# Optimization experiments

Measured on AMD Instinct MI355X. Metric: run time of the kernel, lower is better.

The kernel has to match this reference:

```python
import jax, jax.numpy as jnp
import numpy as np

N_NODES = 100000
N_EDGES = 1600000
HIDDEN = 128
N_LAYERS = 3
N_GRAPHS = 100
EPS = 1e-5


def setup_inputs() -> dict:
    key = jax.random.key(0)
    ks = jax.random.split(key, 9)
    node = jax.random.normal(ks[0], (N_NODES, HIDDEN), dtype=jnp.float32)
    edge_index = jax.random.randint(ks[1], (2, N_EDGES), 0, N_NODES, dtype=jnp.int32)
    edge_attr = jax.random.uniform(ks[2], (N_EDGES,), dtype=jnp.float32)
    batch_ptr = jnp.sort(jax.random.randint(ks[3], (N_NODES,), 0, N_GRAPHS, dtype=jnp.int32))
    W = jax.random.normal(ks[4], (N_LAYERS, HIDDEN, HIDDEN), dtype=jnp.float32) * (1.0 / np.sqrt(HIDDEN))
    b = jax.random.normal(ks[5], (N_LAYERS, HIDDEN), dtype=jnp.float32) * 0.02
    gn_weight = jnp.ones((N_LAYERS, HIDDEN), dtype=jnp.float32)
    gn_bias = jnp.zeros((N_LAYERS, HIDDEN), dtype=jnp.float32)
    gn_alpha = jnp.ones((N_LAYERS, HIDDEN), dtype=jnp.float32)
    return {"node": node, "edge_index": edge_index, "edge_attr": edge_attr,
            "batch_ptr": batch_ptr, "W": W, "b": b, "gn_weight": gn_weight,
            "gn_bias": gn_bias, "gn_alpha": gn_alpha}


def reference(node, edge_index, edge_attr, batch_ptr, W, b, gn_weight, gn_bias, gn_alpha):
    N, d = node.shape
    src, dst = edge_index[0], edge_index[1]
    # GCN normalization with self-loops (weight 1), as in PyG gcn_norm
    loop = jnp.arange(N, dtype=src.dtype)
    src_a = jnp.concatenate([src, loop])
    dst_a = jnp.concatenate([dst, loop])
    w_a = jnp.concatenate([edge_attr, jnp.ones((N,), dtype=edge_attr.dtype)])
    deg = jax.ops.segment_sum(w_a, dst_a, num_segments=N)
    dis = jnp.where(deg > 0, deg ** -0.5, 0.0)
    norm = dis[src_a] * w_a * dis[dst_a]  # [E+N]

    counts = jax.ops.segment_sum(jnp.ones((N,), node.dtype), batch_ptr,
                                 num_segments=N_GRAPHS)[:, None]  # [G,1]

    for l in range(W.shape[0]):
        # GCNConv: linear transform, then gather-normalize-scatter over edges
        h = node @ W[l]  # [N,d]
        agg = jax.ops.segment_sum(norm[:, None] * h[src_a], dst_a, num_segments=N) + b[l]
        # GraphNorm: per-graph mean shift (scaled by alpha) and variance norm
        mean = jax.ops.segment_sum(agg, batch_ptr, num_segments=N_GRAPHS) / counts  # [G,d]
        sub = agg - gn_alpha[l] * mean[batch_ptr]
        var = jax.ops.segment_sum(sub * sub, batch_ptr, num_segments=N_GRAPHS) / counts
        node = jax.nn.relu(gn_weight[l] * sub * jax.lax.rsqrt(var[batch_ptr] + EPS) + gn_bias[l])
    return node
```

## Files before the change

### kernel.cpp

```cpp
#include <hip/hip_runtime.h>
#include <cstdint>

#define N_N 100000
#define N_E 1600000
#define HID 128
#define N_G 100
#define EPSF 1e-5f

#define NB   256
#define EPB  ((N_E + NB - 1) / NB)
#define NBKT ((N_N + 255) >> 8)

static inline int ceil_div(int a, int b){ return (a + b - 1) / b; }

typedef __attribute__((ext_vector_type(8))) short bf16x8;
typedef __attribute__((ext_vector_type(4))) float f32x4;

__device__ inline float bf2f(unsigned short u){
  return __uint_as_float(((unsigned int)u) << 16);
}
__device__ inline unsigned short f2bf(float f){
  unsigned int u = __float_as_uint(f);
  unsigned int r = u + 0x7fffu + ((u >> 16) & 1u);
  return (unsigned short)(r >> 16);
}
__device__ inline void fma8(float* acc, float nv, uint4 u){
  acc[0] += nv * __uint_as_float(u.x << 16);
  acc[1] += nv * __uint_as_float(u.x & 0xffff0000u);
  acc[2] += nv * __uint_as_float(u.y << 16);
  acc[3] += nv * __uint_as_float(u.y & 0xffff0000u);
  acc[4] += nv * __uint_as_float(u.z << 16);
  acc[5] += nv * __uint_as_float(u.z & 0xffff0000u);
  acc[6] += nv * __uint_as_float(u.w << 16);
  acc[7] += nv * __uint_as_float(u.w & 0xffff0000u);
}

__global__ void k_wt3(const float* __restrict__ W, unsigned short* __restrict__ Wt,
                      float* __restrict__ counts, float* __restrict__ sum,
                      float* __restrict__ sumsq){
  int i = blockIdx.x * 256 + threadIdx.x;
  if (i < N_G) counts[i] = 0.0f;
  if (i < N_G * HID){ sum[i] = 0.f; sumsq[i] = 0.f; }
  if (i >= 3 * HID * HID) return;
  int l = i >> 14;
  int r = i & 16383;
  int n = r >> 7, k = r & 127;
  Wt[i] = f2bf(W[l * HID * HID + k * HID + n]);
}

__global__ void k_counts(const int* __restrict__ bp, float* __restrict__ counts){
  int t = blockIdx.x * 256 + threadIdx.x;
  int r0 = t * 32;
  if (r0 >= N_N) return;
  int r1 = min(r0 + 32, N_N);
  int curg = bp[r0];
  float acc = 0.f;
  for (int r = r0; r < r1; ++r){
    int g = bp[r];
    if (g != curg){ atomicAdd(&counts[curg], acc); acc = 0.f; curg = g; }
    acc += 1.0f;
  }
  atomicAdd(&counts[curg], acc);
}

__global__ __launch_bounds__(256) void k_hist(const int* __restrict__ dst,
                                              int* __restrict__ counts){
  __shared__ int h[NBKT];
  int t = threadIdx.x, blk = blockIdx.x;
  for (int i = t; i < NBKT; i += 256) h[i] = 0;
  __syncthreads();
  int e0 = blk * EPB, e1 = min(e0 + EPB, N_E);
  for (int e = e0 + t; e < e1; e += 256)
    atomicAdd(&h[dst[e] >> 8], 1);
  __syncthreads();
  for (int i = t; i < NBKT; i += 256) counts[i * NB + blk] = h[i];
}

__global__ __launch_bounds__(256) void k_scanA(int* __restrict__ data,
                                               int* __restrict__ bsum, int n){
  __shared__ int s[256];
  int t = threadIdx.x;
  int i = blockIdx.x * 256 + t;
  int v = (i < n) ? data[i] : 0;
  s[t] = v; __syncthreads();
  #pragma unroll
  for (int off = 1; off < 256; off <<= 1){
    int tmp = (t >= off) ? s[t - off] : 0;
    __syncthreads();
    s[t] += tmp;
    __syncthreads();
  }
  if (i < n) data[i] = s[t] - v;
  if (t == 255) bsum[blockIdx.x] = s[255];
}

__global__ __launch_bounds__(512) void k_scanB(int* __restrict__ bsum, int nblocks){
  __shared__ int s[512];
  int t = threadIdx.x;
  int v = (t < nblocks) ? bsum[t] : 0;
  s[t] = v; __syncthreads();
  #pragma unroll
  for (int off = 1; off < 512; off <<= 1){
    int tmp = (t >= off) ? s[t - off] : 0;
    __syncthreads();
    s[t] += tmp;
    __syncthreads();
  }
  if (t < nblocks) bsum[t] = s[t] - v;
}

__global__ void k_scanC(int* __restrict__ data, const int* __restrict__ bsum, int n){
  int i = blockIdx.x * 256 + threadIdx.x;
  if (i < n) data[i] += bsum[blockIdx.x];
}

__global__ __launch_bounds__(256) void k_part(const int* __restrict__ src,
                                              const int* __restrict__ dst,
                                              const float* __restrict__ w,
                                              const int* __restrict__ coff,
                                              int2* __restrict__ part){
  __shared__ int off[NBKT];
  int t = threadIdx.x, blk = blockIdx.x;
  for (int i = t; i < NBKT; i += 256) off[i] = coff[i * NB + blk];
  __syncthreads();
  int e0 = blk * EPB, e1 = min(e0 + EPB, N_E);
  for (int e = e0 + t; e < e1; e += 256){
    int d = dst[e];
    int pos = atomicAdd(&off[d >> 8], 1);
    part[pos] = make_int2(src[e] | ((d & 255) << 24), __float_as_int(w[e]));
  }
}

__global__ __launch_bounds__(256) void k_csr(const int* __restrict__ coff,
                                             const int2* __restrict__ part,
                                             int2* __restrict__ edge8,
                                             int* __restrict__ ptr,
                                             float* __restrict__ dis,
                                             float* __restrict__ nself){
  __shared__ int h[256];
  __shared__ int c[256];
  __shared__ float wsum[256];
  __shared__ int s[256];
  int t = threadIdx.x, b = blockIdx.x;
  int base  = coff[b * NB];
  int base2 = (b + 1 < NBKT) ? coff[(b + 1) * NB] : N_E;
  h[t] = 0; c[t] = 0; wsum[t] = 0.f;
  __syncthreads();
  for (int e = base + t; e < base2; e += 256){
    int2 v = part[e];
    int local = ((unsigned int)v.x) >> 24;
    atomicAdd(&h[local], 1);
    atomicAdd(&wsum[local], __int_as_float(v.y));
  }
  __syncthreads();
  int v0 = h[t];
  s[t] = v0; __syncthreads();
  #pragma unroll
  for (int off = 1; off < 256; off <<= 1){
    int tmp = (t >= off) ? s[t - off] : 0;
    __syncthreads();
    s[t] += tmp;
    __syncthreads();
  }
  int mybase = base + s[t] - v0;
  int node = (b << 8) + t;
  float dv = rsqrtf(1.0f + wsum[t]);
  if (node < N_N){
    ptr[node] = mybase;
    dis[node] = dv;
    nself[node] = dv * dv;
  }
  if (b == NBKT - 1 && t == 0) ptr[N_N] = N_E;
  h[t] = mybase;
  __syncthreads();
  wsum[t] = dv;
  __syncthreads();
  for (int e = base + t; e < base2; e += 256){
    int2 v = part[e];
    int local = ((unsigned int)v.x) >> 24;
    int pos = h[local] + atomicAdd(&c[local], 1);
    edge8[pos] = make_int2(v.x & 0x00ffffff,
                           __float_as_int(__int_as_float(v.y) * wsum[local]));
  }
}

__global__ void k_ne(const float* __restrict__ dis, int2* __restrict__ edge8){
  int e = blockIdx.x * 256 + threadIdx.x;
  if (e >= N_E) return;
  int2 v = edge8[e];
  v.y = __float_as_int(__int_as_float(v.y) * dis[v.x]);
  edge8[e] = v;
}

__global__ __launch_bounds__(256) void k_gemm(const float* __restrict__ X,
                                              const float* __restrict__ agg,
                                              int fused,
                                              const int* __restrict__ bp,
                                              const float* __restrict__ mean,
                                              const float* __restrict__ rstd,
                                              const float* __restrict__ alpha,
                                              const float* __restrict__ gwv,
                                              const float* __restrict__ gbv,
                                              const unsigned short* __restrict__ Wt,
                                              unsigned short* __restrict__ Hb, int nrows){
  __shared__ unsigned short lA[64 * 136];
  __shared__ unsigned short lB[128 * 136];
  int tid = threadIdx.x;
  int row0 = blockIdx.x * 64;

  #pragma unroll
  for (int i = 0; i < 8; ++i){
    int c = tid + i * 256;
    int r = c >> 4, cc = c & 15;
    *(uint4*)&lB[r * 136 + cc * 8] = ((const uint4*)Wt)[c];
  }
  #pragma unroll
  for (int i = 0; i < 8; ++i){
    int c = tid + i * 256;
    int r = c >> 5, cc = c & 31;
    int gr = row0 + r;
    float4 v = make_float4(0.f, 0.f, 0.f, 0.f);
    if (gr < nrows){
      if (!fused){
        v = *(const float4*)(X + (size_t)gr * HID + cc * 4);
      } else {
        int g = bp[gr];
        float4 a  = *(const float4*)(agg  + (size_t)gr * HID + cc * 4);
        float4 m  = *(const float4*)(mean + g * HID + cc * 4);
        float4 rs = *(const float4*)(rstd + g * HID + cc * 4);
        float4 al = *(const float4*)(alpha + cc * 4);
        float4 wv = *(const float4*)(gwv + cc * 4);
        float4 bv = *(const float4*)(gbv + cc * 4);
        v.x = fmaxf(wv.x * (a.x - al.x * m.x) * rs.x + bv.x, 0.f);
        v.y = fmaxf(wv.y * (a.y - al.y * m.y) * rs.y + bv.y, 0.f);
        v.z = fmaxf(wv.z * (a.z - al.z * m.z) * rs.z + bv.z, 0.f);
        v.w = fmaxf(wv.w * (a.w - al.w * m.w) * rs.w + bv.w, 0.f);
      }
    }
    unsigned short pk[4] = {f2bf(v.x), f2bf(v.y), f2bf(v.z), f2bf(v.w)};
    *(uint2*)&lA[r * 136 + cc * 4] = *(const uint2*)pk;
  }
  __syncthreads();

  int wave = tid >> 6;
  int lane = tid & 63;
  int l16 = lane & 15;
  int quad = lane >> 4;
  int am = wave * 16 + l16;

  bf16x8 afr[4];
  #pragma unroll
  for (int kc = 0; kc < 4; ++kc)
    afr[kc] = *(const bf16x8*)&lA[am * 136 + kc * 32 + quad * 8];

  #pragma unroll
  for (int nt = 0; nt < 8; ++nt){
    f32x4 acc = {0.f, 0.f, 0.f, 0.f};
    int bn = nt * 16 + l16;
    #pragma unroll
    for (int kc = 0; kc < 4; ++kc){
      bf16x8 bfr = *(const bf16x8*)&lB[bn * 136 + kc * 32 + quad * 8];
      acc = __builtin_amdgcn_mfma_f32_16x16x32_bf16(afr[kc], bfr, acc, 0, 0, 0);
    }
    int gr = row0 + wave * 16 + quad * 4;
    #pragma unroll
    for (int r = 0; r < 4; ++r){
      if (gr + r < nrows)
        Hb[(size_t)(gr + r) * HID + nt * 16 + l16] = f2bf(acc[r]);
    }
  }
}

__global__ __launch_bounds__(256) void k_gather(const int* __restrict__ ptr,
                                                const int2* __restrict__ edge8,
                                                const unsigned short* __restrict__ Hb,
                                                const float* __restrict__ nself,
                                                const float* __restrict__ bias,
                                                float* __restrict__ agg){
  int t = blockIdx.x * 256 + threadIdx.x;
  int node = t >> 4;
  if (node >= N_N) return;
  int lane = t & 15;
  const uint4* h16 = (const uint4*)Hb;
  float ns = nself[node];
  uint4 hu = h16[(size_t)node * 16 + lane];
  float4 b0 = ((const float4*)bias)[lane * 2];
  float4 b1 = ((const float4*)bias)[lane * 2 + 1];
  float acc[8] = {b0.x, b0.y, b0.z, b0.w, b1.x, b1.y, b1.z, b1.w};
  fma8(acc, ns, hu);

  int e0 = ptr[node], e1 = ptr[node + 1];
  int e = e0;
  for (; e + 4 <= e1; e += 4){
    int2 ev0 = edge8[e + 0];
    int2 ev1 = edge8[e + 1];
    int2 ev2 = edge8[e + 2];
    int2 ev3 = edge8[e + 3];
    uint4 r0 = h16[(size_t)ev0.x * 16 + lane];
    uint4 r1 = h16[(size_t)ev1.x * 16 + lane];
    uint4 r2 = h16[(size_t)ev2.x * 16 + lane];
    uint4 r3 = h16[(size_t)ev3.x * 16 + lane];
    fma8(acc, __int_as_float(ev0.y), r0);
    fma8(acc, __int_as_float(ev1.y), r1);
    fma8(acc, __int_as_float(ev2.y), r2);
    fma8(acc, __int_as_float(ev3.y), r3);
  }
  for (; e < e1; ++e){
    int2 ev = edge8[e];
    uint4 r0 = h16[(size_t)ev.x * 16 + lane];
    fma8(acc, __int_as_float(ev.y), r0);
  }
  float4* ap = (float4*)(agg + (size_t)node * HID + lane * 8);
  ap[0] = make_float4(acc[0], acc[1], acc[2], acc[3]);
  ap[1] = make_float4(acc[4], acc[5], acc[6], acc[7]);
}


__global__ __launch_bounds__(128) void k_gstat(const float* __restrict__ agg,
                                               const int* __restrict__ bp,
                                               float* __restrict__ sum,
                                               float* __restrict__ sumsq){
  int f = threadIdx.x;
  int r0 = blockIdx.x * 64;
  int r1 = min(r0 + 64, N_N);
  int curg = bp[r0];
  float s = 0.f, s2 = 0.f;
  for (int r = r0; r < r1; ++r){
    int g = bp[r];
    if (g != curg){
      atomicAdd(&sum[curg * HID + f], s);
      atomicAdd(&sumsq[curg * HID + f], s2);
      s = 0.f; s2 = 0.f; curg = g;
    }
    float v = agg[(size_t)r * HID + f];
    s += v; s2 += v * v;
  }
  atomicAdd(&sum[curg * HID + f], s);
  atomicAdd(&sumsq[curg * HID + f], s2);
}

__global__ void k_finstat(float* __restrict__ sum, float* __restrict__ sumsq,
                          const float* __restrict__ counts, const float* __restrict__ alpha,
                          float* __restrict__ mean, float* __restrict__ rstd){
  int i = blockIdx.x * 256 + threadIdx.x;
  if (i >= N_G * HID) return;
  int f = i & (HID - 1);
  float c = counts[i >> 7];
  float inv = c > 0.f ? 1.0f / c : 0.f;
  float m = sum[i] * inv;
  float ex2 = sumsq[i] * inv;
  float al = alpha[f];
  float var = ex2 - m * m * al * (2.0f - al);
  mean[i] = m;
  rstd[i] = rsqrtf(var + EPSF);
  sum[i] = 0.f;
  sumsq[i] = 0.f;
}

__global__ void k_out(const float* __restrict__ agg, const int* __restrict__ bp,
                      const float* __restrict__ mean, const float* __restrict__ rstd,
                      const float* __restrict__ alpha, const float* __restrict__ gw,
                      const float* __restrict__ gb, float* __restrict__ out){
  int idx = blockIdx.x * 256 + threadIdx.x;
  if (idx >= N_N * 32) return;
  int i = idx >> 5, q = idx & 31;
  int g = bp[i];
  float4 a  = ((const float4*)agg)[idx];
  float4 m  = ((const float4*)mean)[g * 32 + q];
  float4 r  = ((const float4*)rstd)[g * 32 + q];
  float4 al = ((const float4*)alpha)[q];
  float4 wv = ((const float4*)gw)[q];
  float4 bv = ((const float4*)gb)[q];
  float4 o;
  o.x = fmaxf(wv.x * (a.x - al.x * m.x) * r.x + bv.x, 0.f);
  o.y = fmaxf(wv.y * (a.y - al.y * m.y) * r.y + bv.y, 0.f);
  o.z = fmaxf(wv.z * (a.z - al.z * m.z) * r.z + bv.z, 0.f);
  o.w = fmaxf(wv.w * (a.w - al.w * m.w) * r.w + bv.w, 0.f);
  ((float4*)out)[idx] = o;
}


extern "C" void kernel_launch(void* const* d_in, const int* in_sizes, int n_in,
                              void* d_out, int out_size, void* d_ws, size_t ws_size,
                              hipStream_t stream){
  const float* node0 = (const float*)d_in[0];
  const int*   eidx  = (const int*)d_in[1];
  const float* eattr = (const float*)d_in[2];
  const int*   bp    = (const int*)d_in[3];
  const float* W     = (const float*)d_in[4];
  const float* bias  = (const float*)d_in[5];
  const float* gw    = (const float*)d_in[6];
  const float* gb    = (const float*)d_in[7];
  const float* ga    = (const float*)d_in[8];
  float* out = (float*)d_out;
  const int* src = eidx;
  const int* dst = eidx + N_E;

  char* p = (char*)d_ws;
  auto carve = [&](size_t nbytes) -> char* {
    char* q = p; p += (nbytes + 255) & ~(size_t)255; return q;
  };
  float* dis    = (float*)carve((size_t)N_N * 4);
  float* nself  = (float*)carve((size_t)N_N * 4);
  float* counts = (float*)carve((size_t)N_G * 4);
  int*   coff   = (int*)  carve((size_t)NBKT * NB * 4);
  int*   bsum   = (int*)  carve((size_t)512 * 4);
  int*   ptr    = (int*)  carve((size_t)(N_N + 1) * 4);
  int2*  edge8  = (int2*) carve((size_t)N_E * 8);
  unsigned short* hb = (unsigned short*)carve((size_t)N_N * HID * 2);
  unsigned short* wt = (unsigned short*)carve((size_t)3 * HID * HID * 2);
  float* agg    = (float*)carve((size_t)N_N * HID * 4);
  float* mean   = (float*)carve((size_t)N_G * HID * 4);
  float* rstd   = (float*)carve((size_t)N_G * HID * 4);
  float* sum    = (float*)carve((size_t)N_G * HID * 4);
  float* sumsq  = (float*)carve((size_t)N_G * HID * 4);
  int2*  part   = (int2*)agg;

  int nscan = NBKT * NB;
  int nscan_blocks = ceil_div(nscan, 256);

  k_wt3   <<<ceil_div(3 * HID * HID, 256), 256, 0, stream>>>(W, wt, counts, sum, sumsq);
  k_counts<<<ceil_div(N_N, 32 * 256), 256, 0, stream>>>(bp, counts);
  k_hist  <<<NB, 256, 0, stream>>>(dst, coff);
  k_scanA <<<nscan_blocks, 256, 0, stream>>>(coff, bsum, nscan);
  k_scanB <<<1, 512, 0, stream>>>(bsum, nscan_blocks);
  k_scanC <<<nscan_blocks, 256, 0, stream>>>(coff, bsum, nscan);
  k_part  <<<NB, 256, 0, stream>>>(src, dst, eattr, coff, part);
  k_csr   <<<NBKT, 256, 0, stream>>>(coff, part, edge8, ptr, dis, nself);
  k_ne    <<<ceil_div(N_E, 256), 256, 0, stream>>>(dis, edge8);

  for (int l = 0; l < 3; ++l){
    if (l == 0){
      k_gemm <<<ceil_div(N_N, 64), 256, 0, stream>>>(node0, nullptr, 0,
                 nullptr, nullptr, nullptr, nullptr, nullptr, nullptr,
                 wt, hb, N_N);
    } else {
      k_gemm <<<ceil_div(N_N, 64), 256, 0, stream>>>(nullptr, agg, 1,
                 bp, mean, rstd, ga + (l - 1) * HID, gw + (l - 1) * HID,
                 gb + (l - 1) * HID, wt + (size_t)l * HID * HID, hb, N_N);
    }
    k_gather <<<ceil_div(N_N * 16, 256), 256, 0, stream>>>(ptr, edge8, hb, nself,
                 bias + l * HID, agg);
    k_gstat  <<<ceil_div(N_N, 64), 128, 0, stream>>>(agg, bp, sum, sumsq);
    k_finstat<<<ceil_div(N_G * HID, 256), 256, 0, stream>>>(sum, sumsq, counts,
                 ga + l * HID, mean, rstd);
  }
  k_out <<<ceil_div(N_N * 32, 256), 256, 0, stream>>>(agg, bp, mean, rstd,
             ga + 2 * HID, gw + 2 * HID, gb + 2 * HID, out);
}
```

Baseline: 574.5 us.

## Slice H by feature columns per XCC and use persistent atomic-ticket gather

```diff
diff --git a/kernel.cpp b/kernel.cpp
--- a/kernel.cpp
+++ b/kernel.cpp
@@ -11,14 +11,15 @@
 #define EPB  ((N_E + NB - 1) / NB)
 #define NBKT ((N_N + 255) >> 8)
 
+#define NSL  8
+#define CHK  128
+#define NCH  ((N_N + CHK - 1) / CHK)
+
 static inline int ceil_div(int a, int b){ return (a + b - 1) / b; }
 
 typedef __attribute__((ext_vector_type(8))) short bf16x8;
 typedef __attribute__((ext_vector_type(4))) float f32x4;
 
-__device__ inline float bf2f(unsigned short u){
-  return __uint_as_float(((unsigned int)u) << 16);
-}
 __device__ inline unsigned short f2bf(float f){
   unsigned int u = __float_as_uint(f);
   unsigned int r = u + 0x7fffu + ((u >> 16) & 1u);
@@ -35,11 +36,18 @@
   acc[7] += nv * __uint_as_float(u.w & 0xffff0000u);
 }
 
+__device__ inline int get_xcc(){
+  unsigned x;
+  asm volatile("s_getreg_b32 %0, hwreg(HW_REG_XCC_ID)" : "=s"(x));
+  return (int)(x & (NSL - 1));
+}
+
 __global__ void k_wt3(const float* __restrict__ W, unsigned short* __restrict__ Wt,
                       float* __restrict__ counts, float* __restrict__ sum,
-                      float* __restrict__ sumsq){
+                      float* __restrict__ sumsq, int* __restrict__ tick){
   int i = blockIdx.x * 256 + threadIdx.x;
   if (i < N_G) counts[i] = 0.0f;
+  if (i < 3 * NSL) tick[i] = 0;
   if (i < N_G * HID){ sum[i] = 0.f; sumsq[i] = 0.f; }
   if (i >= 3 * HID * HID) return;
   int l = i >> 14;
@@ -263,56 +271,74 @@
       acc = __builtin_amdgcn_mfma_f32_16x16x32_bf16(afr[kc], bfr, acc, 0, 0, 0);
     }
     int gr = row0 + wave * 16 + quad * 4;
+    unsigned short* hbs = Hb + (size_t)nt * ((size_t)N_N * 16);
     #pragma unroll
     for (int r = 0; r < 4; ++r){
       if (gr + r < nrows)
-        Hb[(size_t)(gr + r) * HID + nt * 16 + l16] = f2bf(acc[r]);
-    }
-  }
-}
-
-__global__ __launch_bounds__(256) void k_gather(const int* __restrict__ ptr,
-                                                const int2* __restrict__ edge8,
-                                                const unsigned short* __restrict__ Hb,
-                                                const float* __restrict__ nself,
-                                                const float* __restrict__ bias,
-                                                float* __restrict__ agg){
-  int t = blockIdx.x * 256 + threadIdx.x;
-  int node = t >> 4;
-  if (node >= N_N) return;
-  int lane = t & 15;
-  const uint4* h16 = (const uint4*)Hb;
-  float ns = nself[node];
-  uint4 hu = h16[(size_t)node * 16 + lane];
-  float4 b0 = ((const float4*)bias)[lane * 2];
-  float4 b1 = ((const float4*)bias)[lane * 2 + 1];
-  float acc[8] = {b0.x, b0.y, b0.z, b0.w, b1.x, b1.y, b1.z, b1.w};
-  fma8(acc, ns, hu);
-
-  int e0 = ptr[node], e1 = ptr[node + 1];
-  int e = e0;
-  for (; e + 4 <= e1; e += 4){
-    int2 ev0 = edge8[e + 0];
-    int2 ev1 = edge8[e + 1];
-    int2 ev2 = edge8[e + 2];
-    int2 ev3 = edge8[e + 3];
-    uint4 r0 = h16[(size_t)ev0.x * 16 + lane];
-    uint4 r1 = h16[(size_t)ev1.x * 16 + lane];
-    uint4 r2 = h16[(size_t)ev2.x * 16 + lane];
-    uint4 r3 = h16[(size_t)ev3.x * 16 + lane];
-    fma8(acc, __int_as_float(ev0.y), r0);
-    fma8(acc, __int_as_float(ev1.y), r1);
-    fma8(acc, __int_as_float(ev2.y), r2);
-    fma8(acc, __int_as_float(ev3.y), r3);
-  }
-  for (; e < e1; ++e){
-    int2 ev = edge8[e];
-    uint4 r0 = h16[(size_t)ev.x * 16 + lane];
-    fma8(acc, __int_as_float(ev.y), r0);
-  }
-  float4* ap = (float4*)(agg + (size_t)node * HID + lane * 8);
-  ap[0] = make_float4(acc[0], acc[1], acc[2], acc[3]);
-  ap[1] = make_float4(acc[4], acc[5], acc[6], acc[7]);
+        hbs[(size_t)(gr + r) * 16 + l16] = f2bf(acc[r]);
+    }
+  }
+}
+
+__global__ __launch_bounds__(256, 8) void k_gather(const int* __restrict__ ptr,
+                                                   const int2* __restrict__ edge8,
+                                                   const unsigned short* __restrict__ Hb,
+                                                   const float* __restrict__ nself,
+                                                   const float* __restrict__ bias,
+                                                   float* __restrict__ agg,
+                                                   int* __restrict__ tick){
+  __shared__ int schunk;
+  int myx = get_xcc();
+  int half = threadIdx.x & 1;
+  int trow = threadIdx.x >> 1;
+  const long long* ep = (const long long*)edge8;
+  for (int ss = 0; ss < NSL; ++ss){
+    int s = (myx + ss) & (NSL - 1);
+    const uint4* hs = (const uint4*)(Hb + (size_t)s * ((size_t)N_N * 16));
+    float4 b0 = ((const float4*)bias)[s * 4 + half * 2];
+    float4 b1 = ((const float4*)bias)[s * 4 + half * 2 + 1];
+    for (;;){
+      if (threadIdx.x == 0) schunk = atomicAdd(&tick[s], 1);
+      __syncthreads();
+      int chunk = schunk;
+      __syncthreads();
+      if (chunk >= NCH) break;
+      int node = chunk * CHK + trow;
+      if (node < N_N){
+        float ns = __builtin_nontemporal_load(nself + node);
+        uint4 hu = hs[(size_t)node * 2 + half];
+        float acc[8] = {b0.x, b0.y, b0.z, b0.w, b1.x, b1.y, b1.z, b1.w};
+        fma8(acc, ns, hu);
+        int e0 = __builtin_nontemporal_load(ptr + node);
+        int e1 = __builtin_nontemporal_load(ptr + node + 1);
+        int e = e0;
+        for (; e + 4 <= e1; e += 4){
+          long long v0 = __builtin_nontemporal_load(ep + e + 0);
+          long long v1 = __builtin_nontemporal_load(ep + e + 1);
+          long long v2 = __builtin_nontemporal_load(ep + e + 2);
+          long long v3 = __builtin_nontemporal_load(ep + e + 3);
+          uint4 r0 = hs[(size_t)(unsigned int)v0 * 2 + half];
+          uint4 r1 = hs[(size_t)(unsigned int)v1 * 2 + half];
+          uint4 r2 = hs[(size_t)(unsigned int)v2 * 2 + half];
+          uint4 r3 = hs[(size_t)(unsigned int)v3 * 2 + half];
+          fma8(acc, __uint_as_float((unsigned int)(((unsigned long long)v0) >> 32)), r0);
+          fma8(acc, __uint_as_float((unsigned int)(((unsigned long long)v1) >> 32)), r1);
+          fma8(acc, __uint_as_float((unsigned int)(((unsigned long long)v2) >> 32)), r2);
+          fma8(acc, __uint_as_float((unsigned int)(((unsigned long long)v3) >> 32)), r3);
+        }
+        for (; e < e1; ++e){
+          long long v = __builtin_nontemporal_load(ep + e);
+          uint4 r0 = hs[(size_t)(unsigned int)v * 2 + half];
+          fma8(acc, __uint_as_float((unsigned int)(((unsigned long long)v) >> 32)), r0);
+        }
+        float* ap = agg + (size_t)node * HID + s * 16 + half * 8;
+        f32x4 w0 = {acc[0], acc[1], acc[2], acc[3]};
+        f32x4 w1 = {acc[4], acc[5], acc[6], acc[7]};
+        __builtin_nontemporal_store(w0, (f32x4*)ap);
+        __builtin_nontemporal_store(w1, (f32x4*)ap + 1);
+      }
+    }
+  }
 }
 
 
@@ -406,6 +432,7 @@
   int*   coff   = (int*)  carve((size_t)NBKT * NB * 4);
   int*   bsum   = (int*)  carve((size_t)512 * 4);
   int*   ptr    = (int*)  carve((size_t)(N_N + 1) * 4);
+  int*   tick   = (int*)  carve((size_t)3 * NSL * 4);
   int2*  edge8  = (int2*) carve((size_t)N_E * 8);
   unsigned short* hb = (unsigned short*)carve((size_t)N_N * HID * 2);
   unsigned short* wt = (unsigned short*)carve((size_t)3 * HID * HID * 2);
@@ -419,7 +446,7 @@
   int nscan = NBKT * NB;
   int nscan_blocks = ceil_div(nscan, 256);
 
-  k_wt3   <<<ceil_div(3 * HID * HID, 256), 256, 0, stream>>>(W, wt, counts, sum, sumsq);
+  k_wt3   <<<ceil_div(3 * HID * HID, 256), 256, 0, stream>>>(W, wt, counts, sum, sumsq, tick);
   k_counts<<<ceil_div(N_N, 32 * 256), 256, 0, stream>>>(bp, counts);
   k_hist  <<<NB, 256, 0, stream>>>(dst, coff);
   k_scanA <<<nscan_blocks, 256, 0, stream>>>(coff, bsum, nscan);
@@ -439,8 +466,8 @@
                  bp, mean, rstd, ga + (l - 1) * HID, gw + (l - 1) * HID,
                  gb + (l - 1) * HID, wt + (size_t)l * HID * HID, hb, N_N);
     }
-    k_gather <<<ceil_div(N_N * 16, 256), 256, 0, stream>>>(ptr, edge8, hb, nself,
-                 bias + l * HID, agg);
+    k_gather <<<2048, 256, 0, stream>>>(ptr, edge8, hb, nself,
+                 bias + l * HID, agg, tick + l * NSL);
     k_gstat  <<<ceil_div(N_N, 64), 128, 0, stream>>>(agg, bp, sum, sumsq);
     k_finstat<<<ceil_div(N_G * HID, 256), 256, 0, stream>>>(sum, sumsq, counts,
                  ga + l * HID, mean, rstd);
```

Result: slower. 1.476 ms (+156.9%).

## Replace atomic graph stats with segment-bounded partial sums and fold scan fixup

Applied to the files above, without the earlier changes.

```diff
diff --git a/kernel.cpp b/kernel.cpp
--- a/kernel.cpp
+++ b/kernel.cpp
@@ -16,9 +16,6 @@
 typedef __attribute__((ext_vector_type(8))) short bf16x8;
 typedef __attribute__((ext_vector_type(4))) float f32x4;
 
-__device__ inline float bf2f(unsigned short u){
-  return __uint_as_float(((unsigned int)u) << 16);
-}
 __device__ inline unsigned short f2bf(float f){
   unsigned int u = __float_as_uint(f);
   unsigned int r = u + 0x7fffu + ((u >> 16) & 1u);
@@ -36,11 +33,9 @@
 }
 
 __global__ void k_wt3(const float* __restrict__ W, unsigned short* __restrict__ Wt,
-                      float* __restrict__ counts, float* __restrict__ sum,
-                      float* __restrict__ sumsq){
+                      int* __restrict__ gstart, int* __restrict__ gend){
   int i = blockIdx.x * 256 + threadIdx.x;
-  if (i < N_G) counts[i] = 0.0f;
-  if (i < N_G * HID){ sum[i] = 0.f; sumsq[i] = 0.f; }
+  if (i < N_G){ gstart[i] = 0; gend[i] = 0; }
   if (i >= 3 * HID * HID) return;
   int l = i >> 14;
   int r = i & 16383;
@@ -48,19 +43,13 @@
   Wt[i] = f2bf(W[l * HID * HID + k * HID + n]);
 }
 
-__global__ void k_counts(const int* __restrict__ bp, float* __restrict__ counts){
-  int t = blockIdx.x * 256 + threadIdx.x;
-  int r0 = t * 32;
-  if (r0 >= N_N) return;
-  int r1 = min(r0 + 32, N_N);
-  int curg = bp[r0];
-  float acc = 0.f;
-  for (int r = r0; r < r1; ++r){
-    int g = bp[r];
-    if (g != curg){ atomicAdd(&counts[curg], acc); acc = 0.f; curg = g; }
-    acc += 1.0f;
-  }
-  atomicAdd(&counts[curg], acc);
+__global__ void k_bnd(const int* __restrict__ bp, int* __restrict__ gstart,
+                      int* __restrict__ gend){
+  int i = blockIdx.x * 256 + threadIdx.x;
+  if (i >= N_N) return;
+  int g = bp[i];
+  if (i == 0 || bp[i - 1] != g) gstart[g] = i;
+  if (i == N_N - 1 || bp[i + 1] != g) gend[g] = i + 1;
 }
 
 __global__ __launch_bounds__(256) void k_hist(const int* __restrict__ dst,
@@ -109,19 +98,16 @@
   if (t < nblocks) bsum[t] = s[t] - v;
 }
 
-__global__ void k_scanC(int* __restrict__ data, const int* __restrict__ bsum, int n){
-  int i = blockIdx.x * 256 + threadIdx.x;
-  if (i < n) data[i] += bsum[blockIdx.x];
-}
-
 __global__ __launch_bounds__(256) void k_part(const int* __restrict__ src,
                                               const int* __restrict__ dst,
                                               const float* __restrict__ w,
                                               const int* __restrict__ coff,
+                                              const int* __restrict__ bsum,
                                               int2* __restrict__ part){
   __shared__ int off[NBKT];
   int t = threadIdx.x, blk = blockIdx.x;
-  for (int i = t; i < NBKT; i += 256) off[i] = coff[i * NB + blk];
+  for (int i = t; i < NBKT; i += 256)
+    off[i] = coff[i * NB + blk] + bsum[i];
   __syncthreads();
   int e0 = blk * EPB, e1 = min(e0 + EPB, N_E);
   for (int e = e0 + t; e < e1; e += 256){
@@ -132,6 +118,7 @@
 }
 
 __global__ __launch_bounds__(256) void k_csr(const int* __restrict__ coff,
+                                             const int* __restrict__ bsum,
                                              const int2* __restrict__ part,
                                              int2* __restrict__ edge8,
                                              int* __restrict__ ptr,
@@ -142,8 +129,8 @@
   __shared__ float wsum[256];
   __shared__ int s[256];
   int t = threadIdx.x, b = blockIdx.x;
-  int base  = coff[b * NB];
-  int base2 = (b + 1 < NBKT) ? coff[(b + 1) * NB] : N_E;
+  int base  = coff[b * NB] + bsum[b];
+  int base2 = (b + 1 < NBKT) ? coff[(b + 1) * NB] + bsum[b + 1] : N_E;
   h[t] = 0; c[t] = 0; wsum[t] = 0.f;
   __syncthreads();
   for (int e = base + t; e < base2; e += 256){
@@ -315,46 +302,52 @@
   ap[1] = make_float4(acc[4], acc[5], acc[6], acc[7]);
 }
 
-
-__global__ __launch_bounds__(128) void k_gstat(const float* __restrict__ agg,
-                                               const int* __restrict__ bp,
-                                               float* __restrict__ sum,
-                                               float* __restrict__ sumsq){
-  int f = threadIdx.x;
-  int r0 = blockIdx.x * 64;
-  int r1 = min(r0 + 64, N_N);
-  int curg = bp[r0];
-  float s = 0.f, s2 = 0.f;
-  for (int r = r0; r < r1; ++r){
-    int g = bp[r];
-    if (g != curg){
-      atomicAdd(&sum[curg * HID + f], s);
-      atomicAdd(&sumsq[curg * HID + f], s2);
-      s = 0.f; s2 = 0.f; curg = g;
-    }
+__global__ __launch_bounds__(256) void k_gstat(const float* __restrict__ agg,
+                                               const int* __restrict__ gstart,
+                                               const int* __restrict__ gend,
+                                               float* __restrict__ psum,
+                                               float* __restrict__ psq){
+  __shared__ float ls[256], lq[256];
+  int g = blockIdx.x >> 3, c = blockIdx.x & 7;
+  int s = gstart[g], e = gend[g];
+  int len = e - s;
+  int r0 = s + ((len * c) >> 3);
+  int r1 = s + ((len * (c + 1)) >> 3);
+  int f = threadIdx.x & 127, rr = threadIdx.x >> 7;
+  float sm = 0.f, sq = 0.f;
+  for (int r = r0 + rr; r < r1; r += 2){
     float v = agg[(size_t)r * HID + f];
-    s += v; s2 += v * v;
-  }
-  atomicAdd(&sum[curg * HID + f], s);
-  atomicAdd(&sumsq[curg * HID + f], s2);
-}
-
-__global__ void k_finstat(float* __restrict__ sum, float* __restrict__ sumsq,
-                          const float* __restrict__ counts, const float* __restrict__ alpha,
+    sm += v; sq += v * v;
+  }
+  ls[threadIdx.x] = sm; lq[threadIdx.x] = sq;
+  __syncthreads();
+  if (rr == 0){
+    psum[(size_t)blockIdx.x * HID + f] = ls[f] + ls[f + 128];
+    psq [(size_t)blockIdx.x * HID + f] = lq[f] + lq[f + 128];
+  }
+}
+
+__global__ void k_finstat(const float* __restrict__ psum, const float* __restrict__ psq,
+                          const int* __restrict__ gstart, const int* __restrict__ gend,
+                          const float* __restrict__ alpha,
                           float* __restrict__ mean, float* __restrict__ rstd){
   int i = blockIdx.x * 256 + threadIdx.x;
   if (i >= N_G * HID) return;
-  int f = i & (HID - 1);
-  float c = counts[i >> 7];
+  int g = i >> 7, f = i & (HID - 1);
+  float c = (float)(gend[g] - gstart[g]);
   float inv = c > 0.f ? 1.0f / c : 0.f;
-  float m = sum[i] * inv;
-  float ex2 = sumsq[i] * inv;
+  float sm = 0.f, sq = 0.f;
+  #pragma unroll
+  for (int k = 0; k < 8; ++k){
+    sm += psum[(size_t)(g * 8 + k) * HID + f];
+    sq += psq [(size_t)(g * 8 + k) * HID + f];
+  }
+  float m = sm * inv;
+  float ex2 = sq * inv;
   float al = alpha[f];
   float var = ex2 - m * m * al * (2.0f - al);
   mean[i] = m;
   rstd[i] = rsqrtf(var + EPSF);
-  sum[i] = 0.f;
-  sumsq[i] = 0.f;
 }
 
 __global__ void k_out(const float* __restrict__ agg, const int* __restrict__ bp,
@@ -402,7 +395,8 @@
   };
   float* dis    = (float*)carve((size_t)N_N * 4);
   float* nself  = (float*)carve((size_t)N_N * 4);
-  float* counts = (float*)carve((size_t)N_G * 4);
+  int*   gstart = (int*)  carve((size_t)N_G * 4);
+  int*   gend   = (int*)  carve((size_t)N_G * 4);
   int*   coff   = (int*)  carve((size_t)NBKT * NB * 4);
   int*   bsum   = (int*)  carve((size_t)512 * 4);
   int*   ptr    = (int*)  carve((size_t)(N_N + 1) * 4);
@@ -412,22 +406,21 @@
   float* agg    = (float*)carve((size_t)N_N * HID * 4);
   float* mean   = (float*)carve((size_t)N_G * HID * 4);
   float* rstd   = (float*)carve((size_t)N_G * HID * 4);
-  float* sum    = (float*)carve((size_t)N_G * HID * 4);
-  float* sumsq  = (float*)carve((size_t)N_G * HID * 4);
+  float* psum   = (float*)carve((size_t)N_G * 8 * HID * 4);
+  float* psq    = (float*)carve((size_t)N_G * 8 * HID * 4);
   int2*  part   = (int2*)agg;
 
   int nscan = NBKT * NB;
   int nscan_blocks = ceil_div(nscan, 256);
 
-  k_wt3   <<<ceil_div(3 * HID * HID, 256), 256, 0, stream>>>(W, wt, counts, sum, sumsq);
-  k_counts<<<ceil_div(N_N, 32 * 256), 256, 0, stream>>>(bp, counts);
-  k_hist  <<<NB, 256, 0, stream>>>(dst, coff);
-  k_scanA <<<nscan_blocks, 256, 0, stream>>>(coff, bsum, nscan);
-  k_scanB <<<1, 512, 0, stream>>>(bsum, nscan_blocks);
-  k_scanC <<<nscan_blocks, 256, 0, stream>>>(coff, bsum, nscan);
-  k_part  <<<NB, 256, 0, stream>>>(src, dst, eattr, coff, part);
-  k_csr   <<<NBKT, 256, 0, stream>>>(coff, part, edge8, ptr, dis, nself);
-  k_ne    <<<ceil_div(N_E, 256), 256, 0, stream>>>(dis, edge8);
+  k_wt3  <<<ceil_div(3 * HID * HID, 256), 256, 0, stream>>>(W, wt, gstart, gend);
+  k_bnd  <<<ceil_div(N_N, 256), 256, 0, stream>>>(bp, gstart, gend);
+  k_hist <<<NB, 256, 0, stream>>>(dst, coff);
+  k_scanA<<<nscan_blocks, 256, 0, stream>>>(coff, bsum, nscan);
+  k_scanB<<<1, 512, 0, stream>>>(bsum, nscan_blocks);
+  k_part <<<NB, 256, 0, stream>>>(src, dst, eattr, coff, bsum, part);
+  k_csr  <<<NBKT, 256, 0, stream>>>(coff, bsum, part, edge8, ptr, dis, nself);
+  k_ne   <<<ceil_div(N_E, 256), 256, 0, stream>>>(dis, edge8);
 
   for (int l = 0; l < 3; ++l){
     if (l == 0){
@@ -441,8 +434,8 @@
     }
     k_gather <<<ceil_div(N_N * 16, 256), 256, 0, stream>>>(ptr, edge8, hb, nself,
                  bias + l * HID, agg);
-    k_gstat  <<<ceil_div(N_N, 64), 128, 0, stream>>>(agg, bp, sum, sumsq);
-    k_finstat<<<ceil_div(N_G * HID, 256), 256, 0, stream>>>(sum, sumsq, counts,
+    k_gstat  <<<N_G * 8, 256, 0, stream>>>(agg, gstart, gend, psum, psq);
+    k_finstat<<<ceil_div(N_G * HID, 256), 256, 0, stream>>>(psum, psq, gstart, gend,
                  ga + l * HID, mean, rstd);
   }
   k_out <<<ceil_div(N_N * 32, 256), 256, 0, stream>>>(agg, bp, mean, rstd,
```

Result: faster. 562.0 us (-2.2%).
